# Optimization experiments

Hardware: AMD Instinct MI355X
Metric: run time of the kernel (lower is better)

The kernel has to match this reference:

```python
import jax, jax.numpy as jnp
import numpy as np

B_GRAPHS = 16      # number of graphs in batch
NPG = 8192         # nodes per graph
N = B_GRAPHS * NPG # 131072 total nodes
F_DIM = 64         # node feature dim
K_CLUST = 16       # n_clusters
DEG = 32           # avg degree
E = N * DEG        # 4,194,304 edges


def setup_inputs() -> dict:
    key = jax.random.key(0)
    k1, k2, k3, k4, k5 = jax.random.split(key, 5)
    x = jax.random.normal(k1, (N, F_DIM), jnp.float32)
    W = jax.random.normal(k2, (F_DIM, K_CLUST), jnp.float32) / np.sqrt(F_DIM)
    b = jnp.zeros((K_CLUST,), jnp.float32)
    # edges constrained within each graph -> block-diagonal adjacency (PyG batching)
    g = jnp.repeat(jnp.arange(B_GRAPHS, dtype=jnp.int32), E // B_GRAPHS)
    edge_row = g * NPG + jax.random.randint(k3, (E,), 0, NPG, jnp.int32)
    edge_col = g * NPG + jax.random.randint(k4, (E,), 0, NPG, jnp.int32)
    edge_weight = jax.random.uniform(k5, (E,), jnp.float32)
    return {"x": x, "W": W, "b": b, "edge_weight": edge_weight,
            "edge_row": edge_row, "edge_col": edge_col, "num_graphs": B_GRAPHS}


def _forward(x, W, b, edge_weight, edge_row, edge_col, num_graphs):
    Ntot, Fd = x.shape
    K = W.shape[1]
    Bn = num_graphs
    n = Ntot // Bn  # equal-size graphs (ptr = n * arange(B+1))

    s = x @ W + b                                   # [N,K] cluster logits
    xb = x.reshape(Bn, n, Fd)
    sb = s.reshape(Bn, n, K)
    # out_x = selu(s^T @ x_bd), block b = s_b^T x_b, then hsplit_and_vstack -> [B*K, F]
    out_x = jax.nn.selu(jnp.einsum('bnk,bnf->bkf', sb, xb)).reshape(Bn * K, Fd)

    ss = jax.nn.softmax(s, axis=-1)                 # softmaxed assignments
    ssb = ss.reshape(Bn, n, K)

    # degree d = adj.sum(axis=0)  (column sums over COO edges)
    d = jax.ops.segment_sum(edge_weight, edge_col, num_segments=Ntot)   # [N]
    m2 = d.reshape(Bn, n).sum(1)                    # total degree per graph [B]

    # A @ C via edge scatter: (A C)[row] += w * C[col]
    AC = jax.ops.segment_sum(edge_weight[:, None] * ss[edge_col], edge_row,
                             num_segments=Ntot)     # [N,K]
    # out_adj blocks: C_b^T A_b C_b  -> [B,K,K]
    out_adj = jnp.einsum('bnk,bnl->bkl', ssb, AC.reshape(Bn, n, K))

    # dS_b = C_b^T d_b  (Ca/Cb blocks); normalizer gets m_inv twice in torch code
    dS = jnp.einsum('bn,bnk->bk', d.reshape(Bn, n), ssb)                # [B,K]
    spectral_loss = -jnp.mean(jnp.einsum('bkk->b', out_adj) / m2
                              - (dS ** 2).sum(1) / (m2 ** 2))

    sqrt_K = jnp.sqrt(jnp.float32(K))
    cluster_size = ssb.sum(1)                        # [B,K]
    cluster_loss = jnp.mean(jnp.sqrt((cluster_size ** 2).sum(1)) / n * sqrt_K - 1.0)

    # CC blocks: C_b^T C_b; ortho = mean_b || CC_b/||CC_b||_F - I/sqrt(K) ||_F
    CC = jnp.einsum('bnk,bnl->bkl', ssb, ssb)        # [B,K,K]
    CC_norm = jnp.sqrt((CC ** 2).sum((1, 2)))        # Frobenius norm per block
    eye_div_k = jnp.eye(K, dtype=x.dtype) / sqrt_K
    ortho_loss = jnp.mean(jnp.sqrt(
        ((CC / CC_norm[:, None, None] - eye_div_k) ** 2).sum((1, 2))))

    # mask diagonal and degree-normalize pooled adjacency
    oa = out_adj * (1.0 - jnp.eye(K, dtype=x.dtype))
    dd = jnp.sqrt(oa.sum(2)) + 1e-12                 # row sums per block [B,K]
    out_adj_norm = oa / (dd[:, :, None] * dd[:, None, :])

    return out_x, out_adj_norm, spectral_loss, cluster_loss, ortho_loss


def reference(x, W, b, edge_weight, edge_row, edge_col, num_graphs):
    return _forward(x, W, b, edge_weight, edge_row, edge_col, num_graphs)
```

## Files before the change

kernel.cpp:

```cpp
#include <hip/hip_runtime.h>
#include <math.h>

#define F_DIM 64
#define K_CL 16
#define B_GR 16

typedef _Float16 h16;
using f16x8 = __attribute__((ext_vector_type(8))) _Float16;
using f32x4 = __attribute__((ext_vector_type(4))) float;

__global__ __launch_bounds__(256) void k_assign(
    const float* __restrict__ x, const float* __restrict__ W, const float* __restrict__ bvec,
    float* __restrict__ ss, float* __restrict__ sraw, h16* __restrict__ ssh)
{
    __shared__ float Wl[F_DIM * K_CL];
    __shared__ float bl[K_CL];
    int t = threadIdx.x;
    for (int idx = t; idx < F_DIM * K_CL; idx += 256) Wl[idx] = W[idx];
    if (t < K_CL) bl[t] = bvec[t];
    __syncthreads();

    size_t i = (size_t)blockIdx.x * 256 + t;
    float s[K_CL];
#pragma unroll
    for (int k = 0; k < 16; ++k) s[k] = bl[k];

    const float4* xp = reinterpret_cast<const float4*>(x + i * F_DIM);
#pragma unroll
    for (int j = 0; j < 16; ++j) {
        float4 q = xp[j];
        float xf[4] = {q.x, q.y, q.z, q.w};
#pragma unroll
        for (int ff = 0; ff < 4; ++ff) {
            int f = j * 4 + ff;
            float xv = xf[ff];
            const float4* wr = reinterpret_cast<const float4*>(&Wl[f * K_CL]);
            float4 w0 = wr[0], w1 = wr[1], w2 = wr[2], w3 = wr[3];
            s[0]  += xv * w0.x; s[1]  += xv * w0.y; s[2]  += xv * w0.z; s[3]  += xv * w0.w;
            s[4]  += xv * w1.x; s[5]  += xv * w1.y; s[6]  += xv * w1.z; s[7]  += xv * w1.w;
            s[8]  += xv * w2.x; s[9]  += xv * w2.y; s[10] += xv * w2.z; s[11] += xv * w2.w;
            s[12] += xv * w3.x; s[13] += xv * w3.y; s[14] += xv * w3.z; s[15] += xv * w3.w;
        }
    }

    float4* sp = reinterpret_cast<float4*>(sraw + i * K_CL);
    sp[0] = make_float4(s[0], s[1], s[2], s[3]);
    sp[1] = make_float4(s[4], s[5], s[6], s[7]);
    sp[2] = make_float4(s[8], s[9], s[10], s[11]);
    sp[3] = make_float4(s[12], s[13], s[14], s[15]);

    float m = s[0];
#pragma unroll
    for (int k = 1; k < 16; ++k) m = fmaxf(m, s[k]);
    float sum = 0.f;
#pragma unroll
    for (int k = 0; k < 16; ++k) { s[k] = __expf(s[k] - m); sum += s[k]; }
    float inv = 1.0f / sum;
#pragma unroll
    for (int k = 0; k < 16; ++k) s[k] *= inv;

    float4* qp = reinterpret_cast<float4*>(ss + i * K_CL);
    qp[0] = make_float4(s[0], s[1], s[2], s[3]);
    qp[1] = make_float4(s[4], s[5], s[6], s[7]);
    qp[2] = make_float4(s[8], s[9], s[10], s[11]);
    qp[3] = make_float4(s[12], s[13], s[14], s[15]);

    f16x8 h0, h1;
#pragma unroll
    for (int k = 0; k < 8; ++k) { h0[k] = (h16)s[k]; h1[k] = (h16)s[k + 8]; }
    f16x8* hp = reinterpret_cast<f16x8*>(ssh + i * K_CL);
    hp[0] = h0;
    hp[1] = h1;
}

__global__ __launch_bounds__(256) void k_edge(
    const int* __restrict__ erow, const int* __restrict__ ecol, const float* __restrict__ ew,
    const h16* __restrict__ ssh, float* __restrict__ oadj,
    int edges_per_block, int edges_per_graph, int nmask)
{
    __shared__ float CCl[256];
    int t = threadIdx.x;
    CCl[t] = 0.f;
    __syncthreads();

    int bid = blockIdx.x;
    int xcd = bid & 7;
    int slot = bid >> 3;
    int graph = xcd + 8 * (slot & 1);
    int chunk = slot >> 1;

    int wid = t >> 6, lane = t & 63;
    int quad = lane >> 4, m = lane & 15;

    int epw = edges_per_block >> 2;
    size_t base = (size_t)graph * edges_per_graph
                + (size_t)chunk * edges_per_block
                + (size_t)wid * epw;

    f32x4 acc = {0.f, 0.f, 0.f, 0.f};

    for (int e0 = 0; e0 < epw; e0 += 64) {
        size_t eb = base + e0 + lane;
        int   rv = erow[eb] & nmask;
        int   cv = ecol[eb] & nmask;
        float wv = ew[eb];
#pragma unroll
        for (int h = 0; h < 2; ++h) {
            f16x8 afrag, bfrag;
#pragma unroll
            for (int j = 0; j < 8; ++j) {
                int src = h * 32 + quad * 8 + j;
                int   r = __shfl(rv, src, 64);
                int   c = __shfl(cv, src, 64);
                float w = __shfl(wv, src, 64);
                h16 av = ssh[(size_t)r * 16 + m];
                h16 bv = ssh[(size_t)c * 16 + m];
                afrag[j] = av * (h16)w;
                bfrag[j] = bv;
            }
            acc = __builtin_amdgcn_mfma_f32_16x16x32_f16(afrag, bfrag, acc, 0, 0, 0);
        }
    }

#pragma unroll
    for (int rg = 0; rg < 4; ++rg)
        atomicAdd(&CCl[(quad * 4 + rg) * 16 + m], acc[rg]);
    __syncthreads();
    atomicAdd(oadj + graph * 256 + t, CCl[t]);
}

__global__ __launch_bounds__(256) void k_nodes(
    const float* __restrict__ x, const float* __restrict__ sraw, const float* __restrict__ ss,
    float* __restrict__ outx, float* __restrict__ CCb, float* __restrict__ csb,
    int npw, int npg)
{
    __shared__ float redx[4 * K_CL * F_DIM];
    __shared__ float CCl[256];
    __shared__ float csl[16];
    int t = threadIdx.x;
    CCl[t] = 0.f;
    if (t < 16) csl[t] = 0.f;
    __syncthreads();

    int wid = t >> 6, lane = t & 63;
    int g4 = lane >> 4, l = lane & 15;
    size_t base = ((size_t)blockIdx.x * 4 + wid) * npw;

    float accx[16];
#pragma unroll
    for (int k = 0; k < 16; ++k) accx[k] = 0.f;
    float accc[4] = {0.f, 0.f, 0.f, 0.f};
    float acccs = 0.f;

    for (int j = 0; j < npw; ++j) {
        size_t i = base + j;
        float xv = x[i * F_DIM + lane];
        const float4* sp = reinterpret_cast<const float4*>(sraw + i * K_CL);
        float4 s0 = sp[0], s1 = sp[1], s2 = sp[2], s3 = sp[3];
        accx[0]  += s0.x * xv; accx[1]  += s0.y * xv; accx[2]  += s0.z * xv; accx[3]  += s0.w * xv;
        accx[4]  += s1.x * xv; accx[5]  += s1.y * xv; accx[6]  += s1.z * xv; accx[7]  += s1.w * xv;
        accx[8]  += s2.x * xv; accx[9]  += s2.y * xv; accx[10] += s2.z * xv; accx[11] += s2.w * xv;
        accx[12] += s3.x * xv; accx[13] += s3.y * xv; accx[14] += s3.z * xv; accx[15] += s3.w * xv;

        float sv = ss[i * K_CL + l];
        accc[0] += __shfl(sv, g4 * 4 + 0, 16) * sv;
        accc[1] += __shfl(sv, g4 * 4 + 1, 16) * sv;
        accc[2] += __shfl(sv, g4 * 4 + 2, 16) * sv;
        accc[3] += __shfl(sv, g4 * 4 + 3, 16) * sv;
        acccs += sv;
    }

#pragma unroll
    for (int k = 0; k < 16; ++k) redx[wid * 1024 + k * 64 + lane] = accx[k];
#pragma unroll
    for (int j4 = 0; j4 < 4; ++j4)
        atomicAdd(&CCl[(g4 * 4 + j4) * 16 + l], accc[j4]);
    if (g4 == 0) atomicAdd(&csl[l], acccs);
    __syncthreads();

    int gb = (int)(base / (size_t)npg);
    float* dst = outx + gb * (K_CL * F_DIM);
#pragma unroll
    for (int it = 0; it < 4; ++it) {
        int idx = t + it * 256;
        float v = redx[idx] + redx[1024 + idx] + redx[2048 + idx] + redx[3072 + idx];
        atomicAdd(dst + idx, v);
    }
    atomicAdd(&CCb[gb * 256 + t], CCl[t]);
    if (t < 16) atomicAdd(&csb[gb * 16 + t], csl[t]);
}

__global__ __launch_bounds__(256) void k_final(
    const float* __restrict__ outx, const float* __restrict__ oadj,
    const float* __restrict__ CCb, const float* __restrict__ csb,
    float* __restrict__ out, int npg)
{
    int t = threadIdx.x;
    int gid = blockIdx.x * 256 + t;
    {
        float v = outx[gid];
        float r = (v > 0.f) ? (1.0507009873554805f * v)
                            : (1.0507009873554805f * 1.6732632423543772f * (__expf(v) - 1.0f));
        out[gid] = r;
    }

    if (blockIdx.x != 0) return;

    int b = t >> 4, k = t & 15;
    const float* oar = oadj + b * 256 + k * 16;
    const float* ccr = CCb + b * 256 + k * 16;

    float rowsum_off = 0.f, trace_c = 0.f, rowsum_all = 0.f, fro2 = 0.f, colsum = 0.f;
#pragma unroll
    for (int l = 0; l < 16; ++l) {
        float v = oar[l];
        rowsum_all += v;
        if (l == k) trace_c = v; else rowsum_off += v;
        float c = ccr[l];
        fro2 += c * c;
        colsum += oadj[b * 256 + l * 16 + k];
    }
    float dd = sqrtf(rowsum_off) + 1e-12f;
    __shared__ float ddl[B_GR * K_CL];
    ddl[t] = dd;

    float csv = csb[t];
    float ds2 = colsum * colsum, cs2 = csv * csv;
    float tr = trace_c, m2 = rowsum_all;
#pragma unroll
    for (int msk = 8; msk >= 1; msk >>= 1) {
        tr   += __shfl_xor(tr,   msk, 16);
        ds2  += __shfl_xor(ds2,  msk, 16);
        cs2  += __shfl_xor(cs2,  msk, 16);
        fro2 += __shfl_xor(fro2, msk, 16);
        m2   += __shfl_xor(m2,   msk, 16);
    }
    float invfro = 1.0f / sqrtf(fro2);
    float osum = 0.f;
#pragma unroll
    for (int l = 0; l < 16; ++l) {
        float v = ccr[l] * invfro - ((l == k) ? 0.25f : 0.f);
        osum += v * v;
    }
#pragma unroll
    for (int msk = 8; msk >= 1; msk >>= 1) osum += __shfl_xor(osum, msk, 16);

    __shared__ float sp_s[B_GR], cl_s[B_GR], or_s[B_GR];
    if (k == 0) {
        sp_s[b] = tr / m2 - ds2 / (m2 * m2);
        cl_s[b] = sqrtf(cs2) / (float)npg * 4.0f - 1.0f;
        or_s[b] = sqrtf(osum);
    }
    __syncthreads();
    if (t == 0) {
        float a = 0.f, c = 0.f, o = 0.f;
        for (int i = 0; i < B_GR; ++i) { a += sp_s[i]; c += cl_s[i]; o += or_s[i]; }
        out[20480] = -a / 16.f;
        out[20481] = c / 16.f;
        out[20482] = o / 16.f;
    }

#pragma unroll
    for (int l = 0; l < 16; ++l) {
        float v = (l == k) ? 0.f : oar[l] / (dd * ddl[b * 16 + l]);
        out[16384 + b * 256 + k * 16 + l] = v;
    }
}

extern "C" void kernel_launch(void* const* d_in, const int* in_sizes, int n_in,
                              void* d_out, int out_size, void* d_ws, size_t ws_size,
                              hipStream_t stream)
{
    const float* x    = (const float*)d_in[0];
    const float* W    = (const float*)d_in[1];
    const float* bvec = (const float*)d_in[2];
    const float* ew   = (const float*)d_in[3];
    const int* erow   = (const int*)d_in[4];
    const int* ecol   = (const int*)d_in[5];

    int Ntot = in_sizes[0] / F_DIM;
    size_t E = (size_t)in_sizes[3];
    int npg  = Ntot / B_GR;
    int edges_per_graph = (int)(E / B_GR);
    int nmask = Ntot - 1;

    const int ADJ_BLOCKS  = 2048;
    const int NODE_BLOCKS = 1024;
    int edges_per_block = (int)(E / ADJ_BLOCKS);
    int npw = Ntot / (NODE_BLOCKS * 4);

    char* ws = (char*)d_ws;
    size_t o = 0;
    float* ss    = (float*)(ws + o); o += (size_t)Ntot * 16 * 4;
    float* sraw  = (float*)(ws + o); o += (size_t)Ntot * 16 * 4;
    h16*   ssh   = (h16*)(ws + o);   o += (size_t)Ntot * 16 * 2;
    size_t zoff = o;
    float* outx  = (float*)(ws + o); o += (size_t)B_GR * 1024 * 4;
    float* oadj  = (float*)(ws + o); o += (size_t)B_GR * 256 * 4;
    float* CCb   = (float*)(ws + o); o += (size_t)B_GR * 256 * 4;
    float* csb   = (float*)(ws + o); o += (size_t)B_GR * 16 * 4;

    hipMemsetAsync(ws + zoff, 0, o - zoff, stream);

    k_assign<<<Ntot / 256, 256, 0, stream>>>(x, W, bvec, ss, sraw, ssh);
    k_edge<<<ADJ_BLOCKS, 256, 0, stream>>>(erow, ecol, ew, ssh, oadj,
                                           edges_per_block, edges_per_graph, nmask);
    k_nodes<<<NODE_BLOCKS, 256, 0, stream>>>(x, sraw, ss, outx, CCb, csb, npw, npg);
    k_final<<<64, 256, 0, stream>>>(outx, oadj, CCb, csb, (float*)d_out, npg);
}
```

Measured before the change: 208.6 us.

## Fuse node pooling into assignment kernel with MFMA and vectorize edge gathers

```diff
diff --git a/kernel.cpp b/kernel.cpp
--- a/kernel.cpp
+++ b/kernel.cpp
@@ -4,24 +4,32 @@
 #define F_DIM 64
 #define K_CL 16
 #define B_GR 16
+#define SROW 72
 
 typedef _Float16 h16;
 using f16x8 = __attribute__((ext_vector_type(8))) _Float16;
 using f32x4 = __attribute__((ext_vector_type(4))) float;
 
-__global__ __launch_bounds__(256) void k_assign(
+__global__ __launch_bounds__(256) void k_fused(
     const float* __restrict__ x, const float* __restrict__ W, const float* __restrict__ bvec,
-    float* __restrict__ ss, float* __restrict__ sraw, h16* __restrict__ ssh)
+    h16* __restrict__ ssh, float* __restrict__ outx, float* __restrict__ CCb)
 {
     __shared__ float Wl[F_DIM * K_CL];
     __shared__ float bl[K_CL];
+    __shared__ __align__(16) h16 stage[4][(16 + 16 + 64) * SROW];
+
     int t = threadIdx.x;
     for (int idx = t; idx < F_DIM * K_CL; idx += 256) Wl[idx] = W[idx];
     if (t < K_CL) bl[t] = bvec[t];
     __syncthreads();
 
+    int wid = t >> 6, lane = t & 63;
+    h16* Sg = stage[wid];
+    h16* Cg = Sg + 16 * SROW;
+    h16* Xg = Cg + 16 * SROW;
+
     size_t i = (size_t)blockIdx.x * 256 + t;
-    float s[K_CL];
+    float s[16];
 #pragma unroll
     for (int k = 0; k < 16; ++k) s[k] = bl[k];
 
@@ -34,6 +42,7 @@
         for (int ff = 0; ff < 4; ++ff) {
             int f = j * 4 + ff;
             float xv = xf[ff];
+            Xg[f * SROW + lane] = (h16)xv;
             const float4* wr = reinterpret_cast<const float4*>(&Wl[f * K_CL]);
             float4 w0 = wr[0], w1 = wr[1], w2 = wr[2], w3 = wr[3];
             s[0]  += xv * w0.x; s[1]  += xv * w0.y; s[2]  += xv * w0.z; s[3]  += xv * w0.w;
@@ -43,11 +52,8 @@
         }
     }
 
-    float4* sp = reinterpret_cast<float4*>(sraw + i * K_CL);
-    sp[0] = make_float4(s[0], s[1], s[2], s[3]);
-    sp[1] = make_float4(s[4], s[5], s[6], s[7]);
-    sp[2] = make_float4(s[8], s[9], s[10], s[11]);
-    sp[3] = make_float4(s[12], s[13], s[14], s[15]);
+#pragma unroll
+    for (int k = 0; k < 16; ++k) Sg[k * SROW + lane] = (h16)s[k];
 
     float m = s[0];
 #pragma unroll
@@ -59,18 +65,57 @@
 #pragma unroll
     for (int k = 0; k < 16; ++k) s[k] *= inv;
 
-    float4* qp = reinterpret_cast<float4*>(ss + i * K_CL);
-    qp[0] = make_float4(s[0], s[1], s[2], s[3]);
-    qp[1] = make_float4(s[4], s[5], s[6], s[7]);
-    qp[2] = make_float4(s[8], s[9], s[10], s[11]);
-    qp[3] = make_float4(s[12], s[13], s[14], s[15]);
-
     f16x8 h0, h1;
 #pragma unroll
     for (int k = 0; k < 8; ++k) { h0[k] = (h16)s[k]; h1[k] = (h16)s[k + 8]; }
+#pragma unroll
+    for (int k = 0; k < 8; ++k) {
+        Cg[k * SROW + lane] = h0[k];
+        Cg[(k + 8) * SROW + lane] = h1[k];
+    }
     f16x8* hp = reinterpret_cast<f16x8*>(ssh + i * K_CL);
     hp[0] = h0;
     hp[1] = h1;
+
+    int q4 = lane >> 4, mm = lane & 15;
+    f32x4 accO[4] = {{0.f,0.f,0.f,0.f},{0.f,0.f,0.f,0.f},{0.f,0.f,0.f,0.f},{0.f,0.f,0.f,0.f}};
+    f32x4 accC = {0.f, 0.f, 0.f, 0.f};
+#pragma unroll
+    for (int h = 0; h < 2; ++h) {
+        f16x8 aO = *(const f16x8*)&Sg[mm * SROW + h * 32 + q4 * 8];
+        f16x8 aC = *(const f16x8*)&Cg[mm * SROW + h * 32 + q4 * 8];
+        accC = __builtin_amdgcn_mfma_f32_16x16x32_f16(aC, aC, accC, 0, 0, 0);
+#pragma unroll
+        for (int ft = 0; ft < 4; ++ft) {
+            f16x8 bO = *(const f16x8*)&Xg[(ft * 16 + mm) * SROW + h * 32 + q4 * 8];
+            accO[ft] = __builtin_amdgcn_mfma_f32_16x16x32_f16(aO, bO, accO[ft], 0, 0, 0);
+        }
+    }
+    __syncthreads();
+
+    float* redO = (float*)&stage[0][0];
+    float* redC = redO + 4096;
+#pragma unroll
+    for (int ft = 0; ft < 4; ++ft)
+#pragma unroll
+        for (int rg = 0; rg < 4; ++rg)
+            redO[wid * 1024 + (q4 * 4 + rg) * 64 + ft * 16 + mm] = accO[ft][rg];
+#pragma unroll
+    for (int rg = 0; rg < 4; ++rg)
+        redC[wid * 256 + (q4 * 4 + rg) * 16 + mm] = accC[rg];
+    __syncthreads();
+
+    int g = blockIdx.x >> 5;
+#pragma unroll
+    for (int it = 0; it < 4; ++it) {
+        int idx = t + it * 256;
+        float v = redO[idx] + redO[1024 + idx] + redO[2048 + idx] + redO[3072 + idx];
+        atomicAdd(outx + g * 1024 + idx, v);
+    }
+    {
+        float v = redC[t] + redC[256 + t] + redC[512 + t] + redC[768 + t];
+        atomicAdd(CCb + g * 256 + t, v);
+    }
 }
 
 __global__ __launch_bounds__(256) void k_edge(
@@ -79,6 +124,7 @@
     int edges_per_block, int edges_per_graph, int nmask)
 {
     __shared__ float CCl[256];
+    __shared__ __align__(16) h16 stageE[4][32 * SROW];
     int t = threadIdx.x;
     CCl[t] = 0.f;
     __syncthreads();
@@ -90,110 +136,58 @@
     int chunk = slot >> 1;
 
     int wid = t >> 6, lane = t & 63;
-    int quad = lane >> 4, m = lane & 15;
+    int q4 = lane >> 4, mm = lane & 15;
+    h16* Ag = stageE[wid];
+    h16* Bg = Ag + 16 * SROW;
 
     int epw = edges_per_block >> 2;
     size_t base = (size_t)graph * edges_per_graph
                 + (size_t)chunk * edges_per_block
                 + (size_t)wid * epw;
 
+    const f16x8* sshp = reinterpret_cast<const f16x8*>(ssh);
     f32x4 acc = {0.f, 0.f, 0.f, 0.f};
 
     for (int e0 = 0; e0 < epw; e0 += 64) {
         size_t eb = base + e0 + lane;
-        int   rv = erow[eb] & nmask;
-        int   cv = ecol[eb] & nmask;
-        float wv = ew[eb];
+        int   r = erow[eb] & nmask;
+        int   c = ecol[eb] & nmask;
+        float w = ew[eb];
+
+        f16x8 a0 = sshp[2 * (size_t)r];
+        f16x8 a1 = sshp[2 * (size_t)r + 1];
+        f16x8 b0 = sshp[2 * (size_t)c];
+        f16x8 b1 = sshp[2 * (size_t)c + 1];
+        h16 wh = (h16)w;
+#pragma unroll
+        for (int k = 0; k < 8; ++k) { a0[k] *= wh; a1[k] *= wh; }
+
+#pragma unroll
+        for (int k = 0; k < 8; ++k) {
+            Ag[k * SROW + lane]       = a0[k];
+            Ag[(k + 8) * SROW + lane] = a1[k];
+            Bg[k * SROW + lane]       = b0[k];
+            Bg[(k + 8) * SROW + lane] = b1[k];
+        }
+
 #pragma unroll
         for (int h = 0; h < 2; ++h) {
-            f16x8 afrag, bfrag;
-#pragma unroll
-            for (int j = 0; j < 8; ++j) {
-                int src = h * 32 + quad * 8 + j;
-                int   r = __shfl(rv, src, 64);
-                int   c = __shfl(cv, src, 64);
-                float w = __shfl(wv, src, 64);
-                h16 av = ssh[(size_t)r * 16 + m];
-                h16 bv = ssh[(size_t)c * 16 + m];
-                afrag[j] = av * (h16)w;
-                bfrag[j] = bv;
-            }
-            acc = __builtin_amdgcn_mfma_f32_16x16x32_f16(afrag, bfrag, acc, 0, 0, 0);
+            f16x8 af = *(const f16x8*)&Ag[mm * SROW + h * 32 + q4 * 8];
+            f16x8 bf = *(const f16x8*)&Bg[mm * SROW + h * 32 + q4 * 8];
+            acc = __builtin_amdgcn_mfma_f32_16x16x32_f16(af, bf, acc, 0, 0, 0);
         }
     }
 
 #pragma unroll
     for (int rg = 0; rg < 4; ++rg)
-        atomicAdd(&CCl[(quad * 4 + rg) * 16 + m], acc[rg]);
+        atomicAdd(&CCl[(q4 * 4 + rg) * 16 + mm], acc[rg]);
     __syncthreads();
     atomicAdd(oadj + graph * 256 + t, CCl[t]);
-}
-
-__global__ __launch_bounds__(256) void k_nodes(
-    const float* __restrict__ x, const float* __restrict__ sraw, const float* __restrict__ ss,
-    float* __restrict__ outx, float* __restrict__ CCb, float* __restrict__ csb,
-    int npw, int npg)
-{
-    __shared__ float redx[4 * K_CL * F_DIM];
-    __shared__ float CCl[256];
-    __shared__ float csl[16];
-    int t = threadIdx.x;
-    CCl[t] = 0.f;
-    if (t < 16) csl[t] = 0.f;
-    __syncthreads();
-
-    int wid = t >> 6, lane = t & 63;
-    int g4 = lane >> 4, l = lane & 15;
-    size_t base = ((size_t)blockIdx.x * 4 + wid) * npw;
-
-    float accx[16];
-#pragma unroll
-    for (int k = 0; k < 16; ++k) accx[k] = 0.f;
-    float accc[4] = {0.f, 0.f, 0.f, 0.f};
-    float acccs = 0.f;
-
-    for (int j = 0; j < npw; ++j) {
-        size_t i = base + j;
-        float xv = x[i * F_DIM + lane];
-        const float4* sp = reinterpret_cast<const float4*>(sraw + i * K_CL);
-        float4 s0 = sp[0], s1 = sp[1], s2 = sp[2], s3 = sp[3];
-        accx[0]  += s0.x * xv; accx[1]  += s0.y * xv; accx[2]  += s0.z * xv; accx[3]  += s0.w * xv;
-        accx[4]  += s1.x * xv; accx[5]  += s1.y * xv; accx[6]  += s1.z * xv; accx[7]  += s1.w * xv;
-        accx[8]  += s2.x * xv; accx[9]  += s2.y * xv; accx[10] += s2.z * xv; accx[11] += s2.w * xv;
-        accx[12] += s3.x * xv; accx[13] += s3.y * xv; accx[14] += s3.z * xv; accx[15] += s3.w * xv;
-
-        float sv = ss[i * K_CL + l];
-        accc[0] += __shfl(sv, g4 * 4 + 0, 16) * sv;
-        accc[1] += __shfl(sv, g4 * 4 + 1, 16) * sv;
-        accc[2] += __shfl(sv, g4 * 4 + 2, 16) * sv;
-        accc[3] += __shfl(sv, g4 * 4 + 3, 16) * sv;
-        acccs += sv;
-    }
-
-#pragma unroll
-    for (int k = 0; k < 16; ++k) redx[wid * 1024 + k * 64 + lane] = accx[k];
-#pragma unroll
-    for (int j4 = 0; j4 < 4; ++j4)
-        atomicAdd(&CCl[(g4 * 4 + j4) * 16 + l], accc[j4]);
-    if (g4 == 0) atomicAdd(&csl[l], acccs);
-    __syncthreads();
-
-    int gb = (int)(base / (size_t)npg);
-    float* dst = outx + gb * (K_CL * F_DIM);
-#pragma unroll
-    for (int it = 0; it < 4; ++it) {
-        int idx = t + it * 256;
-        float v = redx[idx] + redx[1024 + idx] + redx[2048 + idx] + redx[3072 + idx];
-        atomicAdd(dst + idx, v);
-    }
-    atomicAdd(&CCb[gb * 256 + t], CCl[t]);
-    if (t < 16) atomicAdd(&csb[gb * 16 + t], csl[t]);
 }
 
 __global__ __launch_bounds__(256) void k_final(
     const float* __restrict__ outx, const float* __restrict__ oadj,
-    const float* __restrict__ CCb, const float* __restrict__ csb,
-    float* __restrict__ out, int npg)
+    const float* __restrict__ CCb, float* __restrict__ out, int npg)
 {
     int t = threadIdx.x;
     int gid = blockIdx.x * 256 + t;
@@ -211,6 +205,7 @@
     const float* ccr = CCb + b * 256 + k * 16;
 
     float rowsum_off = 0.f, trace_c = 0.f, rowsum_all = 0.f, fro2 = 0.f, colsum = 0.f;
+    float csv = 0.f;
 #pragma unroll
     for (int l = 0; l < 16; ++l) {
         float v = oar[l];
@@ -218,13 +213,13 @@
         if (l == k) trace_c = v; else rowsum_off += v;
         float c = ccr[l];
         fro2 += c * c;
+        csv += c;
         colsum += oadj[b * 256 + l * 16 + k];
     }
     float dd = sqrtf(rowsum_off) + 1e-12f;
     __shared__ float ddl[B_GR * K_CL];
     ddl[t] = dd;
 
-    float csv = csb[t];
     float ds2 = colsum * colsum, cs2 = csv * csv;
     float tr = trace_c, m2 = rowsum_all;
 #pragma unroll
@@ -284,27 +279,21 @@
     int edges_per_graph = (int)(E / B_GR);
     int nmask = Ntot - 1;
 
-    const int ADJ_BLOCKS  = 2048;
-    const int NODE_BLOCKS = 1024;
+    const int ADJ_BLOCKS = 2048;
     int edges_per_block = (int)(E / ADJ_BLOCKS);
-    int npw = Ntot / (NODE_BLOCKS * 4);
 
     char* ws = (char*)d_ws;
     size_t o = 0;
-    float* ss    = (float*)(ws + o); o += (size_t)Ntot * 16 * 4;
-    float* sraw  = (float*)(ws + o); o += (size_t)Ntot * 16 * 4;
     h16*   ssh   = (h16*)(ws + o);   o += (size_t)Ntot * 16 * 2;
     size_t zoff = o;
     float* outx  = (float*)(ws + o); o += (size_t)B_GR * 1024 * 4;
     float* oadj  = (float*)(ws + o); o += (size_t)B_GR * 256 * 4;
     float* CCb   = (float*)(ws + o); o += (size_t)B_GR * 256 * 4;
-    float* csb   = (float*)(ws + o); o += (size_t)B_GR * 16 * 4;
 
     hipMemsetAsync(ws + zoff, 0, o - zoff, stream);
 
-    k_assign<<<Ntot / 256, 256, 0, stream>>>(x, W, bvec, ss, sraw, ssh);
+    k_fused<<<Ntot / 256, 256, 0, stream>>>(x, W, bvec, ssh, outx, CCb);
     k_edge<<<ADJ_BLOCKS, 256, 0, stream>>>(erow, ecol, ew, ssh, oadj,
                                            edges_per_block, edges_per_graph, nmask);
-    k_nodes<<<NODE_BLOCKS, 256, 0, stream>>>(x, sraw, ss, outx, CCb, csb, npw, npg);
-    k_final<<<64, 256, 0, stream>>>(outx, oadj, CCb, csb, (float*)d_out, npg);
-}
+    k_final<<<64, 256, 0, stream>>>(outx, oadj, CCb, (float*)d_out, npg);
+}
```

Result: faster. 169.9 us (-18.6%).
